# Kernel tuning notes

Hardware: AMD Instinct MI355X
Metric: run time of the kernel (lower is better)

## Reference

```python
import jax, jax.numpy as jnp
import numpy as np

# Workspace layout constants (match config in init_kwargs)
N_LAYERS = 24
D_MODEL = 2048
D_SPOKE = 128
D_HUB_PRIV = 64
D_HUB_SHARED = 512
D_TAG = 64
D_S_SPOKES = N_LAYERS * D_SPOKE            # 3072
HUB_PRIV_OFF = D_S_SPOKES                  # 3072
HUB_SHARED_OFF = HUB_PRIV_OFF + N_LAYERS * D_HUB_PRIV  # 4608
TAG_OFF = HUB_SHARED_OFF + D_HUB_SHARED    # 5120
D_S = TAG_OFF + N_LAYERS * D_TAG           # 6656
DECAY_WINDOW = 8
B, T = 4, 4096


def setup_inputs() -> dict:
    key = jax.random.key(0)
    ks = jax.random.split(key, 9)
    return {
        "S": jax.random.normal(ks[0], (B, T, D_S), jnp.float32),
        "H": jax.random.normal(ks[1], (B, T, D_MODEL), jnp.float32),
        "w_spoke": jax.random.normal(ks[2], (B, T, D_SPOKE), jnp.float32),
        "w_hub_priv": jax.random.normal(ks[3], (B, T, D_HUB_PRIV), jnp.float32),
        "w_hub_shared": jax.random.normal(ks[4], (B, T, D_HUB_SHARED), jnp.float32),
        "tag": jax.random.normal(ks[5], (B, T, D_TAG), jnp.float32),
        "Wq": jax.random.normal(ks[6], (D_TAG, D_MODEL), jnp.float32) / np.sqrt(D_MODEL).astype(np.float32),
        "Wg": jax.random.normal(ks[7], (D_HUB_SHARED, 2 * D_TAG), jnp.float32) / np.sqrt(2 * D_TAG).astype(np.float32),
        "bg": jnp.zeros((D_HUB_SHARED,), jnp.float32),
        "layer_idx": 12,
    }


def reference(S, H, w_spoke, w_hub_priv, w_hub_shared, tag, Wq, Wg, bg, layer_idx):
    li = int(layer_idx)
    # --- HubDecayGate (layer_idx > 0, decay_window > 0) ---
    start = max(0, li - DECAY_WINDOW)
    n_tags = li - start  # 8
    trs = TAG_OFF + start * D_TAG
    tre = TAG_OFF + li * D_TAG
    # mean over past tags: [B,T,n_tags,d_tag] -> [B,T,d_tag]
    mean_tag = S[:, :, trs:tre].reshape(S.shape[0], S.shape[1], n_tags, D_TAG).mean(axis=2)
    query = jnp.einsum('btm,qm->btq', H, Wq)            # [B,T,d_tag]
    gate_in = jnp.concatenate([query, mean_tag], axis=-1)  # [B,T,2*d_tag]
    gate = jax.nn.sigmoid(jnp.einsum('btk,hk->bth', gate_in, Wg) + bg)  # [B,T,d_hub_shared]
    # gated shared hub (forward of FlooredMultiply is a plain multiply)
    gated_hub = S[:, :, HUB_SHARED_OFF:TAG_OFF] * gate
    S = S.at[:, :, HUB_SHARED_OFF:TAG_OFF].set(gated_hub)
    # --- fused workspace writes ---
    ss = li * D_SPOKE
    hps = HUB_PRIV_OFF + li * D_HUB_PRIV
    ts = TAG_OFF + li * D_TAG
    S = S.at[:, :, ss:ss + D_SPOKE].add(w_spoke)
    S = S.at[:, :, hps:hps + D_HUB_PRIV].add(w_hub_priv)
    S = S.at[:, :, HUB_SHARED_OFF:TAG_OFF].add(w_hub_shared)
    S = S.at[:, :, ts:ts + D_TAG].add(tag)
    return (S, gate)
```

## Files before the change

kernel.cpp:

```cpp
#include <hip/hip_runtime.h>
#include <hip/hip_bf16.h>


#define DM 2048
#define DSZ 6656
#define HUBOFF 4608
#define TAGOFF 5120
#define NTOK 16384
#define DHS 512
#define HSTRIDE 1048

typedef __attribute__((ext_vector_type(8))) short bf16x8;
typedef __attribute__((ext_vector_type(4))) short s16x4;
typedef __attribute__((ext_vector_type(4))) float f32x4;

__device__ __forceinline__ float sigmoidf_(float x) {
  return 1.0f / (1.0f + __expf(-x));
}
__device__ __forceinline__ short f2bf(float x) {
  return (short)__bfloat16_as_ushort(__float2bfloat16(x));
}
__device__ __forceinline__ bf16x8 cvt8(float4 a, float4 b) {
  bf16x8 r;
  r[0] = f2bf(a.x); r[1] = f2bf(a.y); r[2] = f2bf(a.z); r[3] = f2bf(a.w);
  r[4] = f2bf(b.x); r[5] = f2bf(b.y); r[6] = f2bf(b.z); r[7] = f2bf(b.w);
  return r;
}
#define MFMA(a, b, c) __builtin_amdgcn_mfma_f32_16x16x32_bf16((a), (b), (c), 0, 0, 0)

__global__ __launch_bounds__(256) void cw_fused_kernel(
    const float* __restrict__ S, const float* __restrict__ H,
    const float* __restrict__ Wq, const float* __restrict__ Wg,
    const float* __restrict__ bg, const float* __restrict__ whs,
    const float* __restrict__ w_spoke, const float* __restrict__ w_hub_priv,
    const float* __restrict__ tgin, const int* __restrict__ lip,
    float* __restrict__ outS, float* __restrict__ gate_out)
{
  __shared__ float gin[16][132];
  __shared__ __align__(16) char smem[16 * HSTRIDE * 2];
  short (*hds)[HSTRIDE] = (short (*)[HSTRIDE])smem;
  float (*gtile)[516]   = (float (*)[516])smem;

  const int tid = threadIdx.x;
  const int li = *lip;
  const int start = (li > 8) ? (li - 8) : 0;
  const int ntags = li - start;
  const float tscale = (ntags > 0) ? (1.0f / (float)ntags) : 0.0f;
  const int trs = TAGOFF + start * 64;
  const int tok0 = blockIdx.x * 16;
  const int w = tid >> 6, l = tid & 63, l15 = l & 15, l4 = l >> 4;

  const int sp0 = li * 32;
  const int hp0 = 768 + li * 16;
  const int tg0 = 1280 + li * 16;

  const float4* S4 = reinterpret_cast<const float4*>(S);
  const float4* SP4 = reinterpret_cast<const float4*>(w_spoke);
  const float4* HP4 = reinterpret_cast<const float4*>(w_hub_priv);
  const float4* TG4 = reinterpret_cast<const float4*>(tgin);
  float4* O4 = reinterpret_cast<float4*>(outS);

  auto STREAM = [&]() {
    for (int j = 0; j < 6; ++j) {
      const int c = j * 256 + tid;
      const int cp = c + ((c >= 1152) ? 128 : 0);
#pragma unroll
      for (int half = 0; half < 2; ++half) {
        float4 sv[8];
#pragma unroll
        for (int k = 0; k < 8; ++k)
          sv[k] = S4[(size_t)(tok0 + half * 8 + k) * 1664u + cp];
#pragma unroll
        for (int k = 0; k < 8; ++k) {
          const int r = half * 8 + k;
          float4 o = sv[k];
          if (cp >= sp0 && cp < sp0 + 32) {
            float4 v = SP4[(size_t)(tok0 + r) * 32u + (cp - sp0)];
            o.x += v.x; o.y += v.y; o.z += v.z; o.w += v.w;
          } else if (cp >= hp0 && cp < hp0 + 16) {
            float4 v = HP4[(size_t)(tok0 + r) * 16u + (cp - hp0)];
            o.x += v.x; o.y += v.y; o.z += v.z; o.w += v.w;
          } else if (cp >= tg0 && cp < tg0 + 16) {
            float4 v = TG4[(size_t)(tok0 + r) * 16u + (cp - tg0)];
            o.x += v.x; o.y += v.y; o.z += v.z; o.w += v.w;
          }
          O4[(size_t)(tok0 + r) * 1664u + cp] = o;
        }
      }
    }
  };

  auto GATE = [&]() {
    {
      const int tk = tid >> 4, t16 = tid & 15;
      const float4* sp =
          reinterpret_cast<const float4*>(S + (size_t)(tok0 + tk) * DSZ + trs) + t16;
      float4 acc = {0.f, 0.f, 0.f, 0.f};
      for (int g = 0; g < ntags; ++g) {
        float4 v = sp[g * 16];
        acc.x += v.x; acc.y += v.y; acc.z += v.z; acc.w += v.w;
      }
      const int d = 64 + t16 * 4;
      gin[tk][d + 0] = acc.x * tscale;
      gin[tk][d + 1] = acc.y * tscale;
      gin[tk][d + 2] = acc.z * tscale;
      gin[tk][d + 3] = acc.w * tscale;
    }

    const int q0 = w * 16;
    f32x4 qacc = {0.f, 0.f, 0.f, 0.f};
    for (int kc = 0; kc < 2; ++kc) {
      float4 st[16];
      const float* hb = H + (size_t)(tok0 + w * 4) * DM + kc * 1024;
#pragma unroll
      for (int j = 0; j < 16; ++j)
        st[j] = *reinterpret_cast<const float4*>(
            hb + (size_t)(j >> 2) * DM + (j & 3) * 256 + l * 4);
      __syncthreads();
#pragma unroll
      for (int j = 0; j < 16; ++j) {
        s16x4 v;
        v[0] = f2bf(st[j].x); v[1] = f2bf(st[j].y);
        v[2] = f2bf(st[j].z); v[3] = f2bf(st[j].w);
        *reinterpret_cast<s16x4*>(&hds[w * 4 + (j >> 2)][(j & 3) * 256 + l * 4]) = v;
      }
      __syncthreads();
      const float* wqb = Wq + (size_t)(q0 + l15) * DM + kc * 1024 + l4 * 8;
#pragma unroll 4
      for (int ks = 0; ks < 32; ++ks) {
        bf16x8 af = *reinterpret_cast<const bf16x8*>(&hds[l15][ks * 32 + l4 * 8]);
        float4 b0 = *reinterpret_cast<const float4*>(wqb + ks * 32);
        float4 b1 = *reinterpret_cast<const float4*>(wqb + ks * 32 + 4);
        qacc = MFMA(af, cvt8(b0, b1), qacc);
      }
    }
#pragma unroll
    for (int i = 0; i < 4; ++i)
      gin[l4 * 4 + i][q0 + l15] = qacc[i];
    __syncthreads();

    bf16x8 afr[4];
#pragma unroll
    for (int ks = 0; ks < 4; ++ks) {
      const float* p = &gin[l15][ks * 32 + l4 * 8];
      afr[ks] = cvt8(*reinterpret_cast<const float4*>(p),
                     *reinterpret_cast<const float4*>(p + 4));
    }
    const float* wgb = Wg + (size_t)l15 * 128 + l4 * 8;
    for (int jp = 0; jp < 4; ++jp) {
      const int ht0 = w * 8 + jp * 2;
      const float* wp0 = wgb + (size_t)ht0 * 16 * 128;
      const float* wp1 = wp0 + 16 * 128;
      float4 r0[4][2], r1[4][2];
#pragma unroll
      for (int ks = 0; ks < 4; ++ks) {
        r0[ks][0] = *reinterpret_cast<const float4*>(wp0 + ks * 32);
        r0[ks][1] = *reinterpret_cast<const float4*>(wp0 + ks * 32 + 4);
        r1[ks][0] = *reinterpret_cast<const float4*>(wp1 + ks * 32);
        r1[ks][1] = *reinterpret_cast<const float4*>(wp1 + ks * 32 + 4);
      }
      f32x4 accA = {0.f,0.f,0.f,0.f}, accB = {0.f,0.f,0.f,0.f};
#pragma unroll
      for (int ks = 0; ks < 4; ++ks) {
        accA = MFMA(afr[ks], cvt8(r0[ks][0], r0[ks][1]), accA);
        accB = MFMA(afr[ks], cvt8(r1[ks][0], r1[ks][1]), accB);
      }
#pragma unroll
      for (int t = 0; t < 2; ++t) {
        const f32x4 a = t ? accB : accA;
        const int h = (ht0 + t) * 16 + l15;
        const float bgv = bg[h];
#pragma unroll
        for (int i = 0; i < 4; ++i)
          gtile[l4 * 4 + i][h] = sigmoidf_(a[i] + bgv);
      }
    }
    __syncthreads();

#pragma unroll
    for (int r2 = 0; r2 < 8; ++r2) {
      const int idx = r2 * 256 + tid;
      const int row = idx >> 7, qq = idx & 127;
      const int tok = tok0 + row;
      float4 g = *reinterpret_cast<const float4*>(&gtile[row][qq * 4]);
      float4 s = *reinterpret_cast<const float4*>(S + (size_t)tok * DSZ + HUBOFF + qq * 4);
      float4 wv = *reinterpret_cast<const float4*>(whs + (size_t)tok * DHS + qq * 4);
      float4 o;
      o.x = s.x * g.x + wv.x;
      o.y = s.y * g.y + wv.y;
      o.z = s.z * g.z + wv.z;
      o.w = s.w * g.w + wv.w;
      *reinterpret_cast<float4*>(outS + (size_t)tok * DSZ + HUBOFF + qq * 4) = o;
      *reinterpret_cast<float4*>(gate_out + (size_t)tok * DHS + qq * 4) = g;
    }
  };

  if (blockIdx.x & 1) { GATE(); STREAM(); }
  else                { STREAM(); GATE(); }
}

extern "C" void kernel_launch(void* const* d_in, const int* in_sizes, int n_in,
                              void* d_out, int out_size, void* d_ws, size_t ws_size,
                              hipStream_t stream) {
  (void)in_sizes; (void)n_in; (void)out_size; (void)d_ws; (void)ws_size;
  const float* S            = (const float*)d_in[0];
  const float* H            = (const float*)d_in[1];
  const float* w_spoke      = (const float*)d_in[2];
  const float* w_hub_priv   = (const float*)d_in[3];
  const float* w_hub_shared = (const float*)d_in[4];
  const float* tgin         = (const float*)d_in[5];
  const float* Wq           = (const float*)d_in[6];
  const float* Wg           = (const float*)d_in[7];
  const float* bg           = (const float*)d_in[8];
  const int*   lip          = (const int*)d_in[9];

  float* outS = (float*)d_out;
  float* gate_out = outS + (size_t)NTOK * DSZ;

  cw_fused_kernel<<<1024, 256, 0, stream>>>(
      S, H, Wq, Wg, bg, w_hub_shared, w_spoke, w_hub_priv, tgin, lip,
      outS, gate_out);
}
```

Baseline: 246.5 us.

## Warp-specialize block: separate stream and gate warpgroups, load H directly

Blocks grow to 512 threads: the upper four waves do the plain copy and add stream of S, while the lower four waves compute the gate. The H-to-bf16 LDS staging is dropped; each lane now loads H fragments straight from global memory into the MFMA. This lets the bandwidth-bound copy and the compute-heavy gate overlap inside one block and removes an LDS round trip. In exchange H rows are read with a less coalesced pattern, and the stream waves must issue matching dummy __syncthreads calls, which is fragile and may stall them.

```diff
diff --git a/kernel.cpp b/kernel.cpp
--- a/kernel.cpp
+++ b/kernel.cpp
@@ -8,10 +8,8 @@
 #define TAGOFF 5120
 #define NTOK 16384
 #define DHS 512
-#define HSTRIDE 1048
 
 typedef __attribute__((ext_vector_type(8))) short bf16x8;
-typedef __attribute__((ext_vector_type(4))) short s16x4;
 typedef __attribute__((ext_vector_type(4))) float f32x4;
 
 __device__ __forceinline__ float sigmoidf_(float x) {
@@ -28,7 +26,7 @@
 }
 #define MFMA(a, b, c) __builtin_amdgcn_mfma_f32_16x16x32_bf16((a), (b), (c), 0, 0, 0)
 
-__global__ __launch_bounds__(256) void cw_fused_kernel(
+__global__ __launch_bounds__(512) void cw_fused_kernel(
     const float* __restrict__ S, const float* __restrict__ H,
     const float* __restrict__ Wq, const float* __restrict__ Wg,
     const float* __restrict__ bg, const float* __restrict__ whs,
@@ -37,9 +35,7 @@
     float* __restrict__ outS, float* __restrict__ gate_out)
 {
   __shared__ float gin[16][132];
-  __shared__ __align__(16) char smem[16 * HSTRIDE * 2];
-  short (*hds)[HSTRIDE] = (short (*)[HSTRIDE])smem;
-  float (*gtile)[516]   = (float (*)[516])smem;
+  __shared__ float gtile[16][516];
 
   const int tid = threadIdx.x;
   const int li = *lip;
@@ -48,7 +44,8 @@
   const float tscale = (ntags > 0) ? (1.0f / (float)ntags) : 0.0f;
   const int trs = TAGOFF + start * 64;
   const int tok0 = blockIdx.x * 16;
-  const int w = tid >> 6, l = tid & 63, l15 = l & 15, l4 = l >> 4;
+  const int w = tid >> 6;
+  const int l = tid & 63, l15 = l & 15, l4 = l >> 4;
 
   const int sp0 = li * 32;
   const int hp0 = 768 + li * 16;
@@ -60,9 +57,10 @@
   const float4* TG4 = reinterpret_cast<const float4*>(tgin);
   float4* O4 = reinterpret_cast<float4*>(outS);
 
-  auto STREAM = [&]() {
+  if (w >= 4) {
+    const int stid = tid - 256;
     for (int j = 0; j < 6; ++j) {
-      const int c = j * 256 + tid;
+      const int c = j * 256 + stid;
       const int cp = c + ((c >= 1152) ? 128 : 0);
 #pragma unroll
       for (int half = 0; half < 2; ++half) {
@@ -88,9 +86,9 @@
         }
       }
     }
-  };
-
-  auto GATE = [&]() {
+    __syncthreads();
+    __syncthreads();
+  } else {
     {
       const int tk = tid >> 4, t16 = tid & 15;
       const float4* sp =
@@ -108,35 +106,22 @@
     }
 
     const int q0 = w * 16;
-    f32x4 qacc = {0.f, 0.f, 0.f, 0.f};
-    for (int kc = 0; kc < 2; ++kc) {
-      float4 st[16];
-      const float* hb = H + (size_t)(tok0 + w * 4) * DM + kc * 1024;
-#pragma unroll
-      for (int j = 0; j < 16; ++j)
-        st[j] = *reinterpret_cast<const float4*>(
-            hb + (size_t)(j >> 2) * DM + (j & 3) * 256 + l * 4);
-      __syncthreads();
-#pragma unroll
-      for (int j = 0; j < 16; ++j) {
-        s16x4 v;
-        v[0] = f2bf(st[j].x); v[1] = f2bf(st[j].y);
-        v[2] = f2bf(st[j].z); v[3] = f2bf(st[j].w);
-        *reinterpret_cast<s16x4*>(&hds[w * 4 + (j >> 2)][(j & 3) * 256 + l * 4]) = v;
-      }
-      __syncthreads();
-      const float* wqb = Wq + (size_t)(q0 + l15) * DM + kc * 1024 + l4 * 8;
+    {
+      const float* ha = H + (size_t)(tok0 + l15) * DM + l4 * 8;
+      const float* wq = Wq + (size_t)(q0 + l15) * DM + l4 * 8;
+      f32x4 qacc = {0.f, 0.f, 0.f, 0.f};
 #pragma unroll 4
-      for (int ks = 0; ks < 32; ++ks) {
-        bf16x8 af = *reinterpret_cast<const bf16x8*>(&hds[l15][ks * 32 + l4 * 8]);
-        float4 b0 = *reinterpret_cast<const float4*>(wqb + ks * 32);
-        float4 b1 = *reinterpret_cast<const float4*>(wqb + ks * 32 + 4);
-        qacc = MFMA(af, cvt8(b0, b1), qacc);
-      }
-    }
-#pragma unroll
-    for (int i = 0; i < 4; ++i)
-      gin[l4 * 4 + i][q0 + l15] = qacc[i];
+      for (int ks = 0; ks < 64; ++ks) {
+        float4 a0 = *reinterpret_cast<const float4*>(ha + ks * 32);
+        float4 a1 = *reinterpret_cast<const float4*>(ha + ks * 32 + 4);
+        float4 b0 = *reinterpret_cast<const float4*>(wq + ks * 32);
+        float4 b1 = *reinterpret_cast<const float4*>(wq + ks * 32 + 4);
+        qacc = MFMA(cvt8(a0, a1), cvt8(b0, b1), qacc);
+      }
+#pragma unroll
+      for (int i = 0; i < 4; ++i)
+        gin[l4 * 4 + i][q0 + l15] = qacc[i];
+    }
     __syncthreads();
 
     bf16x8 afr[4];
@@ -193,10 +178,7 @@
       *reinterpret_cast<float4*>(outS + (size_t)tok * DSZ + HUBOFF + qq * 4) = o;
       *reinterpret_cast<float4*>(gate_out + (size_t)tok * DHS + qq * 4) = g;
     }
-  };
-
-  if (blockIdx.x & 1) { GATE(); STREAM(); }
-  else                { STREAM(); GATE(); }
+  }
 }
 
 extern "C" void kernel_launch(void* const* d_in, const int* in_sizes, int n_in,
@@ -217,7 +199,7 @@
   float* outS = (float*)d_out;
   float* gate_out = outS + (size_t)NTOK * DSZ;
 
-  cw_fused_kernel<<<1024, 256, 0, stream>>>(
+  cw_fused_kernel<<<1024, 512, 0, stream>>>(
       S, H, Wq, Wg, bg, w_hub_shared, w_spoke, w_hub_priv, tgin, lip,
       outS, gate_out);
 }
```

After: 287.8 us. 16.7% more time.
